# Performance work log

Measured on AMD Instinct MI355X. Metric: run time of the kernel, lower is better.

The kernel has to match this reference:

```python
import jax, jax.numpy as jnp
import numpy as np

TEMPERATURE = 0.1

def setup_inputs() -> dict:
    key = jax.random.key(0)
    k1, k2 = jax.random.split(key)
    z_i = jax.random.normal(k1, (4096, 128), dtype=jnp.float32)
    z_j = jax.random.normal(k2, (4096, 128), dtype=jnp.float32)
    return {"z_i": z_i, "z_j": z_j}

def reference(z_i, z_j):
    n = z_i.shape[0]
    reps = jnp.concatenate([z_i, z_j], axis=0)              # (2N, D)
    # cosine similarity via normalize + GEMM (same math as broadcasted CosineSimilarity,
    # torch eps=1e-8 on the norm)
    norms = jnp.maximum(jnp.linalg.norm(reps, axis=1, keepdims=True), 1e-8)
    rn = reps / norms
    sim = rn @ rn.T                                          # (2N, 2N)
    l_pos = jnp.diagonal(sim, offset=n)                      # (N,)
    r_pos = jnp.diagonal(sim, offset=-n)                     # (N,)
    positives = jnp.concatenate([l_pos, r_pos])[:, None]     # (2N, 1)
    # NOTE: original code's mask bug makes `negatives` the FULL sim matrix
    logits = jnp.concatenate([positives, sim], axis=1) / TEMPERATURE  # (2N, 2N+1)
    # cross-entropy with label 0, reduction='sum'
    log_probs = jax.nn.log_softmax(logits, axis=1)
    loss = -jnp.sum(log_probs[:, 0])
    return loss / (2 * n)
```

## Files before the change

### kernel.cpp

```cpp
#include <hip/hip_runtime.h>
#include <hip/hip_bf16.h>

typedef float f32x4 __attribute__((ext_vector_type(4)));

#define NROWS 8192
#define HALF_N 4096
#define DIM 128
#define C1 14.42695040888963f
#define LN2 0.6931471805599453f
#define GBLK 1024


__global__ __launch_bounds__(256) void k_normalize(
    const float* __restrict__ zi, const float* __restrict__ zj,
    char* __restrict__ packA, char* __restrict__ packB,
    float* __restrict__ rowsum, float* __restrict__ pbuf,
    unsigned int* __restrict__ done)
{
    const int wave = threadIdx.x >> 6;
    const int lane = threadIdx.x & 63;
    const int ks_  = lane >> 4;
    const int qr_  = (lane >> 2) & 3;
    const int rem_ = (lane & 3) * 2;
    #pragma unroll
    for (int t = 0; t < 2; ++t) {
        const int idx = blockIdx.x * 8 + wave * 2 + t;
        float2 vi = *(const float2*)(zi + (size_t)idx * DIM + lane * 2);
        float2 vj = *(const float2*)(zj + (size_t)idx * DIM + lane * 2);
        float ssi = vi.x * vi.x + vi.y * vi.y;
        float ssj = vj.x * vj.x + vj.y * vj.y;
        float cr  = vi.x * vj.x + vi.y * vj.y;
        #pragma unroll
        for (int m = 32; m >= 1; m >>= 1) {
            ssi += __shfl_xor(ssi, m, 64);
            ssj += __shfl_xor(ssj, m, 64);
            cr  += __shfl_xor(cr,  m, 64);
        }
        const float sci = 1.0f / fmaxf(sqrtf(ssi), 1e-8f);
        const float scj = 1.0f / fmaxf(sqrtf(ssj), 1e-8f);
        #pragma unroll
        for (int h = 0; h < 2; ++h) {
            const int   row = idx + h * HALF_N;
            const float sx  = h ? vj.x * scj : vi.x * sci;
            const float sy  = h ? vj.y * scj : vi.y * sci;
            const size_t off = (size_t)(row >> 4) * 2048 + ks_ * 512
                             + (qr_ * 16 + (row & 15)) * 8 + rem_;
            unsigned ua = __builtin_amdgcn_cvt_pk_fp8_f32(sx * C1, sy * C1, 0, false);
            unsigned ub = __builtin_amdgcn_cvt_pk_fp8_f32(sx,      sy,      0, false);
            *(unsigned short*)(packA + off) = (unsigned short)ua;
            *(unsigned short*)(packB + off) = (unsigned short)ub;
        }
        if (lane == 0) {
            const float p = cr * sci * scj;
            pbuf[idx] = p;
            pbuf[idx + HALF_N] = p;
        }
    }
    if (threadIdx.x < 16) rowsum[blockIdx.x * 16 + threadIdx.x] = 0.0f;
    if (blockIdx.x == 0 && threadIdx.x == 0) *done = 0u;
}

__global__ __launch_bounds__(256, 2) void k_gemm(
    const char* __restrict__ packA, const char* __restrict__ packB,
    float* __restrict__ rowsum, const float* __restrict__ pbuf,
    unsigned int* __restrict__ done, float* __restrict__ out)
{
    const int wave = threadIdx.x >> 6;
    const int lane = threadIdx.x & 63;
    const int qrow = lane >> 4, lcol = lane & 15;
    const int cv = blockIdx.x & 31;
    const int rg = (blockIdx.x >> 5) * 4 + wave;

    long afrag[4][4];
    #pragma unroll
    for (int mi = 0; mi < 4; ++mi)
        #pragma unroll
        for (int ks = 0; ks < 4; ++ks)
            afrag[mi][ks] = *(const long*)(packA
                + (size_t)(rg * 4 + mi) * 2048 + ks * 512 + lane * 8);

    float rsum[4][4];
    #pragma unroll
    for (int mi = 0; mi < 4; ++mi)
        #pragma unroll
        for (int r = 0; r < 4; ++r) rsum[mi][r] = 0.0f;

    const char* Bb = packB + (size_t)(cv * 16) * 2048 + lane * 8;

    #pragma unroll 4
    for (int s = 0; s < 16; ++s) {
        const char* bp = Bb + (size_t)s * 2048;
        long bfrag[4];
        #pragma unroll
        for (int ks = 0; ks < 4; ++ks)
            bfrag[ks] = *(const long*)(bp + ks * 512);

        f32x4 acc[4];
        const f32x4 zero = {0.0f, 0.0f, 0.0f, 0.0f};
        #pragma unroll
        for (int mi = 0; mi < 4; ++mi) acc[mi] = zero;
        #pragma unroll
        for (int ks = 0; ks < 4; ++ks)
            #pragma unroll
            for (int mi = 0; mi < 4; ++mi)
                acc[mi] = __builtin_amdgcn_mfma_f32_16x16x32_fp8_fp8(
                    afrag[mi][ks], bfrag[ks], acc[mi], 0, 0, 0);

        #pragma unroll
        for (int mi = 0; mi < 4; ++mi)
            #pragma unroll
            for (int r = 0; r < 4; ++r)
                rsum[mi][r] += __builtin_amdgcn_exp2f(acc[mi][r]);
    }

    #pragma unroll
    for (int mi = 0; mi < 4; ++mi)
        #pragma unroll
        for (int r = 0; r < 4; ++r) {
            float v = rsum[mi][r];
            v += __shfl_xor(v, 1, 64);
            v += __shfl_xor(v, 2, 64);
            v += __shfl_xor(v, 4, 64);
            v += __shfl_xor(v, 8, 64);
            if (lcol == 0)
                atomicAdd(&rowsum[rg * 64 + mi * 16 + qrow * 4 + r], v);
        }

    __syncthreads();
    __shared__ int is_last;
    if (threadIdx.x == 0) {
        unsigned old = __hip_atomic_fetch_add(done, 1u, __ATOMIC_RELAXED,
                                              __HIP_MEMORY_SCOPE_AGENT);
        is_last = (old == GBLK - 1);
    }
    __syncthreads();
    if (!is_last) return;
    __threadfence();

    float lsum = 0.0f;
    for (int r = threadIdx.x; r < NROWS; r += 256) {
        float rs = __hip_atomic_load(&rowsum[r], __ATOMIC_RELAXED, __HIP_MEMORY_SCOPE_AGENT);
        float pc = pbuf[r] * C1;
        float S  = rs + __builtin_amdgcn_exp2f(pc);
        lsum += (__builtin_amdgcn_logf(S) - pc) * LN2;
    }
    #pragma unroll
    for (int m = 32; m >= 1; m >>= 1) lsum += __shfl_xor(lsum, m, 64);
    __shared__ float part[4];
    if (lane == 0) part[wave] = lsum;
    __syncthreads();
    if (threadIdx.x == 0)
        out[0] = (part[0] + part[1] + part[2] + part[3]) * (1.0f / (float)NROWS);
}

extern "C" void kernel_launch(void* const* d_in, const int* in_sizes, int n_in,
                              void* d_out, int out_size, void* d_ws, size_t ws_size,
                              hipStream_t stream)
{
    const float* zi = (const float*)d_in[0];
    const float* zj = (const float*)d_in[1];
    float* out = (float*)d_out;

    char*  packA  = (char*)d_ws;
    char*  packB  = packA + (size_t)NROWS * 128;
    float* rowsum = (float*)(packB + (size_t)NROWS * 128);
    float* pbuf   = rowsum + NROWS;
    unsigned int* done = (unsigned int*)(pbuf + NROWS);

    k_normalize<<<NROWS / 16, 256, 0, stream>>>(zi, zj, packA, packB, rowsum, pbuf, done);
    k_gemm<<<GBLK, 256, 0, stream>>>(packA, packB, rowsum, pbuf, done, out);
}
```

Before: 93.52 us.

## Exploit similarity-matrix symmetry to compute only the upper-triangular tiles

```diff
diff --git a/kernel.cpp b/kernel.cpp
--- a/kernel.cpp
+++ b/kernel.cpp
@@ -8,7 +8,8 @@
 #define DIM 128
 #define C1 14.42695040888963f
 #define LN2 0.6931471805599453f
-#define GBLK 1024
+#define NSTRIP 2112
+#define GBLK (NSTRIP / 4)
 
 
 __global__ __launch_bounds__(256) void k_normalize(
@@ -68,8 +69,17 @@
     const int wave = threadIdx.x >> 6;
     const int lane = threadIdx.x & 63;
     const int qrow = lane >> 4, lcol = lane & 15;
-    const int cv = blockIdx.x & 31;
-    const int rg = (blockIdx.x >> 5) * 4 + wave;
+
+    const int s_id = blockIdx.x * 4 + wave;
+    int q = (int)((130.0f - sqrtf(16900.0f - 8.0f * (float)s_id)) * 0.25f);
+    while (130 * (q + 1) - 2 * (q + 1) * (q + 1) <= s_id) ++q;
+    while (130 * q - 2 * q * q > s_id) --q;
+    const int rem = s_id - (130 * q - 2 * q * q);
+    const int w   = 32 - q;
+    const int rg  = 4 * q + rem / w;
+    const int cv  = q + rem % w;
+    const int diag = (cv == q);
+    const int d0   = diag ? ((rg & 3) * 4) : 0;
 
     long afrag[4][4];
     #pragma unroll
@@ -88,7 +98,7 @@
     const char* Bb = packB + (size_t)(cv * 16) * 2048 + lane * 8;
 
     #pragma unroll 4
-    for (int s = 0; s < 16; ++s) {
+    for (int s = d0; s < 16; ++s) {
         const char* bp = Bb + (size_t)s * 2048;
         long bfrag[4];
         #pragma unroll
@@ -106,11 +116,21 @@
                 acc[mi] = __builtin_amdgcn_mfma_f32_16x16x32_fp8_fp8(
                     afrag[mi][ks], bfrag[ks], acc[mi], 0, 0, 0);
 
+        float cs = 0.0f;
         #pragma unroll
         for (int mi = 0; mi < 4; ++mi)
             #pragma unroll
-            for (int r = 0; r < 4; ++r)
-                rsum[mi][r] += __builtin_amdgcn_exp2f(acc[mi][r]);
+            for (int r = 0; r < 4; ++r) {
+                const float e = __builtin_amdgcn_exp2f(acc[mi][r]);
+                rsum[mi][r] += e;
+                cs += e;
+            }
+        if (!diag || s >= d0 + 4) {
+            cs += __shfl_xor(cs, 16, 64);
+            cs += __shfl_xor(cs, 32, 64);
+            if (qrow == 0)
+                atomicAdd(&rowsum[cv * 256 + s * 16 + lcol], cs);
+        }
     }
 
     #pragma unroll
```

New measurement: 91.13 us, median of 2. 2.6% less time.
